# Kernel tuning notes

Hardware: AMD Instinct MI355X
Metric: run time of the kernel (lower is better)

## Reference

```python
import jax, jax.numpy as jnp
import numpy as np

D_MODEL = 1024
N_HEADS = 16
D_K = D_MODEL // N_HEADS


def setup_inputs() -> dict:
    key = jax.random.key(0)
    ks = jax.random.split(key, 11)
    B, S = 4, 2048
    scale = 1.0 / np.sqrt(D_MODEL)
    inp = {
        "Q": jax.random.normal(ks[0], (B, S, D_MODEL), jnp.float32),
        "K": jax.random.normal(ks[1], (B, S, D_MODEL), jnp.float32),
        "V": jax.random.normal(ks[2], (B, S, D_MODEL), jnp.float32),
        "Wq": jax.random.normal(ks[3], (D_MODEL, D_MODEL), jnp.float32) * scale,
        "bq": jnp.zeros((D_MODEL,), jnp.float32),
        "Wk": jax.random.normal(ks[4], (D_MODEL, D_MODEL), jnp.float32) * scale,
        "bk": jnp.zeros((D_MODEL,), jnp.float32),
        "Wv": jax.random.normal(ks[5], (D_MODEL, D_MODEL), jnp.float32) * scale,
        "bv": jnp.zeros((D_MODEL,), jnp.float32),
        "Wo": jax.random.normal(ks[6], (D_MODEL, D_MODEL), jnp.float32) * scale,
        "bo": jnp.zeros((D_MODEL,), jnp.float32),
    }
    return inp


def _split_heads(x):
    B, S, _ = x.shape
    return x.reshape(B, S, N_HEADS, D_K).transpose(0, 2, 1, 3)  # [B,H,S,Dk]


def reference(Q, K, V, Wq, bq, Wk, bk, Wv, bv, Wo, bo):
    # torch nn.Linear: y = x @ W.T + b
    q = _split_heads(Q @ Wq.T + bq)
    k = _split_heads(K @ Wk.T + bk)
    v = _split_heads(V @ Wv.T + bv)
    scores = jnp.einsum("bhsd,bhtd->bhst", q, k) / jnp.sqrt(jnp.float32(D_K))
    probs = jax.nn.softmax(scores, axis=-1)
    attn = jnp.einsum("bhst,bhtd->bhsd", probs, v)  # [B,H,S,Dk]
    B, H, S, Dk = attn.shape
    combined = attn.transpose(0, 2, 1, 3).reshape(B, S, H * Dk)
    return combined @ Wo.T + bo
```

## Files before the change

kernel.cpp:

```cpp
#include <hip/hip_runtime.h>
#include <hip/hip_bf16.h>

typedef float  f32x4  __attribute__((ext_vector_type(4)));
typedef float  f32x16 __attribute__((ext_vector_type(16)));
typedef float  fvec4  __attribute__((ext_vector_type(4)));
typedef __bf16 bf16x8 __attribute__((ext_vector_type(8)));
typedef unsigned short u16x4 __attribute__((ext_vector_type(4)));
typedef unsigned short u16x8 __attribute__((ext_vector_type(8)));
typedef unsigned int   u32x4 __attribute__((ext_vector_type(4)));

#define DEVINL __device__ __forceinline__

constexpr int D_MODEL = 1024;
constexpr int NH      = 16;
constexpr int DK      = 64;
constexpr int SEQ     = 2048;
constexpr int BATCH   = 4;
constexpr int M_TOK   = BATCH * SEQ;

DEVINL unsigned short f32_to_bf16_u(float f) {
    unsigned int u = __builtin_bit_cast(unsigned int, f);
    u = (u + 0x7FFFu + ((u >> 16) & 1u)) >> 16;
    return (unsigned short)u;
}

DEVINL float exp2_fast(float x) { return __builtin_amdgcn_exp2f(x); }

DEVINL unsigned cvt_pk_bf16(float lo, float hi_) {
    unsigned d;
    asm("v_cvt_pk_bf16_f32 %0, %1, %2" : "=v"(d) : "v"(lo), "v"(hi_));
    return d;
}

DEVINL int vperm_s(int s0) { return (s0 & ~12) | ((s0 & 4) << 1) | ((s0 & 8) >> 1); }

__global__ __launch_bounds__(256) void cvt4(const float* __restrict__ a,
                                            const float* __restrict__ b,
                                            const float* __restrict__ c,
                                            const float* __restrict__ d,
                                            unsigned short* __restrict__ dst, int n8)
{
    int y = blockIdx.y;
    const float* s = (y == 0) ? a : (y == 1) ? b : (y == 2) ? c : d;
    size_t i = blockIdx.x * 256 + threadIdx.x;
    fvec4 v0 = *reinterpret_cast<const fvec4*>(s + i * 8);
    fvec4 v1 = *reinterpret_cast<const fvec4*>(s + i * 8 + 4);
    bf16x8 o;
    #pragma unroll
    for (int j = 0; j < 4; ++j) { o[j] = (__bf16)v0[j]; o[j + 4] = (__bf16)v1[j]; }
    *reinterpret_cast<bf16x8*>(dst + ((size_t)y * n8 + i) * 8) = o;
}

__global__ __launch_bounds__(256) void gemm_qkv(
    const float* __restrict__ Qi, const float* __restrict__ Ki,
    const float* __restrict__ Vi,
    const unsigned short* __restrict__ wq, const unsigned short* __restrict__ wk,
    const unsigned short* __restrict__ wv,
    const float* __restrict__ bq, const float* __restrict__ bk,
    const float* __restrict__ bv,
    unsigned short* __restrict__ qo, unsigned short* __restrict__ ko,
    unsigned short* __restrict__ vo, float qscale)
{
    constexpr int K = D_MODEL;
    constexpr int BUF = 128 * 64 * 2;
    __shared__ char As_[BUF * 2];
    __shared__ char Bs_[BUF * 2];

    const int y = blockIdx.y;
    const float* Ap = (y == 0) ? Qi : (y == 1) ? Ki : Vi;
    const unsigned short* Wb = (y == 0) ? wq : (y == 1) ? wk : wv;
    const float* bias = (y == 0) ? bq : (y == 1) ? bk : bv;

    const int tid  = threadIdx.x;
    const int lane = tid & 63;
    const int wave = tid >> 6;
    const int wr = (wave >> 1) * 64;
    const int wc = (wave & 1) * 64;
    const int wg = ((int)blockIdx.x & 7) * 64 + ((int)blockIdx.x >> 3);
    const int n0 = (wg & 7) * 128;
    const int m0 = (wg >> 3) * 128;
    const int l15 = lane & 15, h16 = lane >> 4;

    f32x4 acc[4][4] = {};
    fvec4 ar[4][2];
    u16x8 wr_[4];

    #pragma unroll
    for (int i = 0; i < 4; ++i) {
        int chunk = tid + i * 256;
        int r = chunk >> 3, c16 = chunk & 7;
        const float* src = Ap + (size_t)(m0 + r) * K + c16 * 8;
        ar[i][0] = *reinterpret_cast<const fvec4*>(src);
        ar[i][1] = *reinterpret_cast<const fvec4*>(src + 4);
        wr_[i] = *reinterpret_cast<const u16x8*>(Wb + (size_t)(n0 + r) * K + c16 * 8);
    }
    #pragma unroll
    for (int i = 0; i < 4; ++i) {
        int chunk = tid + i * 256;
        int r = chunk >> 3;
        bf16x8 o;
        #pragma unroll
        for (int j = 0; j < 4; ++j) { o[j] = (__bf16)ar[i][0][j]; o[j + 4] = (__bf16)ar[i][1][j]; }
        int boff = (chunk * 16) ^ ((r & 7) << 4);
        *reinterpret_cast<bf16x8*>(As_ + boff) = o;
        *reinterpret_cast<u16x8*>(Bs_ + boff) = wr_[i];
    }
    __syncthreads();

    int curb = 0;
    for (int kt = 0; kt < K; kt += 64) {
        if (kt + 64 < K) {
            #pragma unroll
            for (int i = 0; i < 4; ++i) {
                int chunk = tid + i * 256;
                int r = chunk >> 3, c16 = chunk & 7;
                const float* src = Ap + (size_t)(m0 + r) * K + (kt + 64) + c16 * 8;
                ar[i][0] = *reinterpret_cast<const fvec4*>(src);
                ar[i][1] = *reinterpret_cast<const fvec4*>(src + 4);
                wr_[i] = *reinterpret_cast<const u16x8*>(Wb + (size_t)(n0 + r) * K + (kt + 64) + c16 * 8);
            }
        }

        const char* Ar = As_ + curb * BUF;
        const char* Br = Bs_ + curb * BUF;
        #pragma unroll
        for (int kk = 0; kk < 2; ++kk) {
            bf16x8 af[4], bfr[4];
            #pragma unroll
            for (int mi = 0; mi < 4; ++mi) {
                int r = wr + mi * 16 + l15;
                af[mi] = *reinterpret_cast<const bf16x8*>(
                    Ar + ((r * 128 + kk * 64 + h16 * 16) ^ ((r & 7) << 4)));
            }
            #pragma unroll
            for (int ni = 0; ni < 4; ++ni) {
                int r = wc + ni * 16 + l15;
                bfr[ni] = *reinterpret_cast<const bf16x8*>(
                    Br + ((r * 128 + kk * 64 + h16 * 16) ^ ((r & 7) << 4)));
            }
            #pragma unroll
            for (int mi = 0; mi < 4; ++mi)
                #pragma unroll
                for (int ni = 0; ni < 4; ++ni)
                    acc[mi][ni] = __builtin_amdgcn_mfma_f32_16x16x32_bf16(
                        af[mi], bfr[ni], acc[mi][ni], 0, 0, 0);
        }

        if (kt + 64 < K) {
            char* Aw = As_ + (curb ^ 1) * BUF;
            char* Bw = Bs_ + (curb ^ 1) * BUF;
            #pragma unroll
            for (int i = 0; i < 4; ++i) {
                int chunk = tid + i * 256;
                int r = chunk >> 3;
                bf16x8 o;
                #pragma unroll
                for (int j = 0; j < 4; ++j) { o[j] = (__bf16)ar[i][0][j]; o[j + 4] = (__bf16)ar[i][1][j]; }
                int boff = (chunk * 16) ^ ((r & 7) << 4);
                *reinterpret_cast<bf16x8*>(Aw + boff) = o;
                *reinterpret_cast<u16x8*>(Bw + boff) = wr_[i];
            }
        }
        __syncthreads();
        curb ^= 1;
    }

    const int rl = h16 * 4;
    #pragma unroll
    for (int mi = 0; mi < 4; ++mi) {
        #pragma unroll
        for (int ni = 0; ni < 4; ++ni) {
            int col = n0 + wc + ni * 16 + l15;
            float bv_ = bias[col];
            if (y == 2) {
                int row0 = m0 + wr + mi * 16 + rl;
                int bb = row0 >> 11, s0 = row0 & (SEQ - 1);
                int sp = vperm_s(s0);
                int h = col >> 6, dk = col & (DK - 1);
                u16x4 o;
                #pragma unroll
                for (int r = 0; r < 4; ++r)
                    o[r] = f32_to_bf16_u(acc[mi][ni][r] + bv_);
                *reinterpret_cast<u16x4*>(vo +
                    (((size_t)bb * NH + h) * DK + dk) * SEQ + sp) = o;
            } else {
                float sc = (y == 0) ? qscale : 1.0f;
                unsigned short* op = (y == 0) ? qo : ko;
                #pragma unroll
                for (int r = 0; r < 4; ++r) {
                    int row = m0 + wr + mi * 16 + rl + r;
                    int bb = row >> 11, s = row & (SEQ - 1);
                    int h = col >> 6, dk = col & (DK - 1);
                    op[((((size_t)bb * NH + h) * SEQ) + s) * DK + dk]
                        = f32_to_bf16_u((acc[mi][ni][r] + bv_) * sc);
                }
            }
        }
    }
}

__global__ __launch_bounds__(256) void gemm_obf(const unsigned short* __restrict__ Ap,
                                                const unsigned short* __restrict__ Wb,
                                                const float* __restrict__ bias,
                                                float* __restrict__ outp)
{
    constexpr int K = D_MODEL, N = D_MODEL;
    constexpr int BUF = 128 * 64 * 2;
    __shared__ char As_[BUF * 2];
    __shared__ char Bs_[BUF * 2];

    const int tid  = threadIdx.x;
    const int lane = tid & 63;
    const int wave = tid >> 6;
    const int wr = (wave >> 1) * 64;
    const int wc = (wave & 1) * 64;
    const int wg = ((int)blockIdx.x & 7) * 64 + ((int)blockIdx.x >> 3);
    const int n0 = (wg & 7) * 128;
    const int m0 = (wg >> 3) * 128;
    const int l15 = lane & 15, h16 = lane >> 4;

    f32x4 acc[4][4] = {};
    u16x8 areg[4], wreg[4];

    #pragma unroll
    for (int i = 0; i < 4; ++i) {
        int chunk = tid + i * 256;
        int r = chunk >> 3, c16 = chunk & 7;
        areg[i] = *reinterpret_cast<const u16x8*>(Ap + (size_t)(m0 + r) * K + c16 * 8);
        wreg[i] = *reinterpret_cast<const u16x8*>(Wb + (size_t)(n0 + r) * K + c16 * 8);
    }
    #pragma unroll
    for (int i = 0; i < 4; ++i) {
        int chunk = tid + i * 256;
        int r = chunk >> 3;
        int boff = (chunk * 16) ^ ((r & 7) << 4);
        *reinterpret_cast<u16x8*>(As_ + boff) = areg[i];
        *reinterpret_cast<u16x8*>(Bs_ + boff) = wreg[i];
    }
    __syncthreads();

    int curb = 0;
    for (int kt = 0; kt < K; kt += 64) {
        if (kt + 64 < K) {
            #pragma unroll
            for (int i = 0; i < 4; ++i) {
                int chunk = tid + i * 256;
                int r = chunk >> 3, c16 = chunk & 7;
                areg[i] = *reinterpret_cast<const u16x8*>(Ap + (size_t)(m0 + r) * K + (kt + 64) + c16 * 8);
                wreg[i] = *reinterpret_cast<const u16x8*>(Wb + (size_t)(n0 + r) * K + (kt + 64) + c16 * 8);
            }
        }

        const char* Ar = As_ + curb * BUF;
        const char* Br = Bs_ + curb * BUF;
        #pragma unroll
        for (int kk = 0; kk < 2; ++kk) {
            bf16x8 af[4], bfr[4];
            #pragma unroll
            for (int mi = 0; mi < 4; ++mi) {
                int r = wr + mi * 16 + l15;
                af[mi] = *reinterpret_cast<const bf16x8*>(
                    Ar + ((r * 128 + kk * 64 + h16 * 16) ^ ((r & 7) << 4)));
            }
            #pragma unroll
            for (int ni = 0; ni < 4; ++ni) {
                int r = wc + ni * 16 + l15;
                bfr[ni] = *reinterpret_cast<const bf16x8*>(
                    Br + ((r * 128 + kk * 64 + h16 * 16) ^ ((r & 7) << 4)));
            }
            #pragma unroll
            for (int mi = 0; mi < 4; ++mi)
                #pragma unroll
                for (int ni = 0; ni < 4; ++ni)
                    acc[mi][ni] = __builtin_amdgcn_mfma_f32_16x16x32_bf16(
                        af[mi], bfr[ni], acc[mi][ni], 0, 0, 0);
        }

        if (kt + 64 < K) {
            char* Aw = As_ + (curb ^ 1) * BUF;
            char* Bw = Bs_ + (curb ^ 1) * BUF;
            #pragma unroll
            for (int i = 0; i < 4; ++i) {
                int chunk = tid + i * 256;
                int r = chunk >> 3;
                int boff = (chunk * 16) ^ ((r & 7) << 4);
                *reinterpret_cast<u16x8*>(Aw + boff) = areg[i];
                *reinterpret_cast<u16x8*>(Bw + boff) = wreg[i];
            }
        }
        __syncthreads();
        curb ^= 1;
    }

    const int rl = h16 * 4;
    #pragma unroll
    for (int mi = 0; mi < 4; ++mi) {
        #pragma unroll
        for (int ni = 0; ni < 4; ++ni) {
            int col = n0 + wc + ni * 16 + l15;
            float bv = bias[col];
            #pragma unroll
            for (int r = 0; r < 4; ++r) {
                int row = m0 + wr + mi * 16 + rl + r;
                outp[(size_t)row * N + col] = acc[mi][ni][r] + bv;
            }
        }
    }
}

__global__ __launch_bounds__(512, 4) void attn_kernel(const unsigned short* __restrict__ qb,
                                                      const unsigned short* __restrict__ kb,
                                                      const unsigned short* __restrict__ vt,
                                                      unsigned short* __restrict__ ob)
{
    __shared__ char lds[32768];

    const int tid  = threadIdx.x;
    const int lane = tid & 63;
    const int tl31 = lane & 31;
    const int hi   = lane >> 5;
    const int wave = tid >> 6;
    const int wg   = ((int)blockIdx.x & 7) * 64 + ((int)blockIdx.x >> 3);
    const int bh   = wg >> 3;
    const int q0   = (wg & 7) * 256;
    const size_t base  = (size_t)bh * SEQ * DK;
    const size_t baseT = (size_t)bh * DK * SEQ;

    const int k_kt = tid >> 8, k_kd = (tid >> 6) & 3, k_hi = (tid >> 5) & 1, k_tl = tid & 31;
    const size_t k_goff = base + (size_t)(k_kt * 32 + k_tl) * DK + k_kd * 16 + k_hi * 8;
    const int v_tg = tid >> 6, v_dh = (tid >> 5) & 1, v_dl = tid & 31;
    const size_t v_goff = baseT + (size_t)(v_dh * 32 + v_dl) * SEQ + v_tg * 8;

    bf16x8 qf[4];
    #pragma unroll
    for (int kd = 0; kd < 4; ++kd)
        qf[kd] = *reinterpret_cast<const bf16x8*>(
            qb + base + (size_t)(q0 + wave * 32 + tl31) * DK + kd * 16 + hi * 8);

    f32x16 oaccT[2] = {};
    float l_run = 0.f;

    {
        u16x8 kreg = *reinterpret_cast<const u16x8*>(kb + k_goff);
        u16x8 vreg = *reinterpret_cast<const u16x8*>(vt + v_goff);
        *reinterpret_cast<u16x8*>(lds + tid * 16) = kreg;
        *reinterpret_cast<u16x8*>(lds + 8192 + tid * 16) = vreg;
    }
    __syncthreads();

    for (int t = 0; t < 32; ++t) {
        const int cur = t & 1;
        const char* Kr = lds + cur * 16384;
        const char* Vr = Kr + 8192;

        u16x8 kreg, vreg;
        if (t < 31) {
            const int t0n = (t + 1) * 64;
            kreg = *reinterpret_cast<const u16x8*>(kb + k_goff + (size_t)t0n * DK);
            vreg = *reinterpret_cast<const u16x8*>(vt + v_goff + t0n);
        }

        f32x16 sT[2] = {};
        __builtin_amdgcn_s_setprio(1);
        #pragma unroll
        for (int kt = 0; kt < 2; ++kt)
            #pragma unroll
            for (int kd = 0; kd < 4; ++kd) {
                bf16x8 kf = *reinterpret_cast<const bf16x8*>(Kr + kt * 4096 + kd * 1024 + lane * 16);
                sT[kt] = __builtin_amdgcn_mfma_f32_32x32x16_bf16(kf, qf[kd], sT[kt], 0, 0, 0);
            }
        __builtin_amdgcn_s_setprio(0);

        {
            float rs0 = 0.f, rs1 = 0.f, rs2 = 0.f, rs3 = 0.f;
            #pragma unroll
            for (int kt = 0; kt < 2; ++kt)
                #pragma unroll
                for (int i = 0; i < 16; i += 4) {
                    float p0 = exp2_fast(sT[kt][i + 0]);
                    float p1 = exp2_fast(sT[kt][i + 1]);
                    float p2 = exp2_fast(sT[kt][i + 2]);
                    float p3 = exp2_fast(sT[kt][i + 3]);
                    sT[kt][i + 0] = p0; sT[kt][i + 1] = p1;
                    sT[kt][i + 2] = p2; sT[kt][i + 3] = p3;
                    rs0 += p0; rs1 += p1; rs2 += p2; rs3 += p3;
                }
            float rs = (rs0 + rs1) + (rs2 + rs3);
            rs += __shfl_xor(rs, 32);
            l_run += rs;
        }

        __builtin_amdgcn_s_setprio(1);
        #pragma unroll
        for (int ks = 0; ks < 4; ++ks) {
            bf16x8 vfA0 = *reinterpret_cast<const bf16x8*>(Vr + ks * 2048 + hi * 1024 + tl31 * 16);
            bf16x8 vfA1 = *reinterpret_cast<const bf16x8*>(Vr + ks * 2048 + hi * 1024 + 512 + tl31 * 16);
            const int kt = ks >> 1, r0 = (ks & 1) * 8;
            u32x4 w;
            w[0] = cvt_pk_bf16(sT[kt][r0 + 0], sT[kt][r0 + 1]);
            w[1] = cvt_pk_bf16(sT[kt][r0 + 2], sT[kt][r0 + 3]);
            w[2] = cvt_pk_bf16(sT[kt][r0 + 4], sT[kt][r0 + 5]);
            w[3] = cvt_pk_bf16(sT[kt][r0 + 6], sT[kt][r0 + 7]);
            bf16x8 pa = __builtin_bit_cast(bf16x8, w);
            oaccT[0] = __builtin_amdgcn_mfma_f32_32x32x16_bf16(vfA0, pa, oaccT[0], 0, 0, 0);
            oaccT[1] = __builtin_amdgcn_mfma_f32_32x32x16_bf16(vfA1, pa, oaccT[1], 0, 0, 0);
        }
        __builtin_amdgcn_s_setprio(0);

        if (t < 31) {
            char* Kw = lds + (cur ^ 1) * 16384;
            *reinterpret_cast<u16x8*>(Kw + tid * 16) = kreg;
            *reinterpret_cast<u16x8*>(Kw + 8192 + tid * 16) = vreg;
        }
        __syncthreads();
    }

    char* myregion = lds + wave * 4096;
    const int bb = bh >> 4, h = bh & 15;
    {
        float rl = 1.0f / l_run;
        #pragma unroll
        for (int dh = 0; dh < 2; ++dh)
            #pragma unroll
            for (int r = 0; r < 16; ++r) {
                int dl = (r & 3) + 8 * (r >> 2) + 4 * hi + 32 * dh;
                int boff = (tl31 * 128 + dl * 2) ^ ((tl31 & 7) << 4);
                *reinterpret_cast<unsigned short*>(myregion + boff) =
                    f32_to_bf16_u(oaccT[dh][r] * rl);
            }
        #pragma unroll
        for (int c = 0; c < 4; ++c) {
            int chunk = lane + c * 64;
            int row = chunk >> 3, c16 = chunk & 7;
            int boff = (row * 128 + c16 * 16) ^ ((row & 7) << 4);
            u16x8 v = *reinterpret_cast<const u16x8*>(myregion + boff);
            size_t tok = (size_t)(bb * SEQ) + q0 + wave * 32 + row;
            *reinterpret_cast<u16x8*>(ob + tok * D_MODEL + h * DK + c16 * 8) = v;
        }
    }
}

extern "C" void kernel_launch(void* const* d_in, const int* in_sizes, int n_in,
                              void* d_out, int out_size, void* d_ws, size_t ws_size,
                              hipStream_t stream)
{
    const float* Q  = (const float*)d_in[0];
    const float* K_ = (const float*)d_in[1];
    const float* V  = (const float*)d_in[2];
    const float* Wq = (const float*)d_in[3];
    const float* bq = (const float*)d_in[4];
    const float* Wk = (const float*)d_in[5];
    const float* bk = (const float*)d_in[6];
    const float* Wv = (const float*)d_in[7];
    const float* bv = (const float*)d_in[8];
    const float* Wo = (const float*)d_in[9];
    const float* bo = (const float*)d_in[10];
    float* out = (float*)d_out;

    const size_t SZ = (size_t)M_TOK * D_MODEL;
    const size_t WZ = (size_t)D_MODEL * D_MODEL;
    unsigned short* qh_ = (unsigned short*)d_ws;
    unsigned short* kh_ = qh_ + SZ;
    unsigned short* vh_ = kh_ + SZ;
    unsigned short* ah_ = vh_ + SZ;
    unsigned short* wqb = ah_ + SZ;
    unsigned short* wkb = wqb + WZ;
    unsigned short* wvb = wkb + WZ;
    unsigned short* wob = wvb + WZ;

    const float qscale = 0.125f * 1.4426950408889634f;

    cvt4<<<dim3((int)(WZ / 8 / 256), 4), 256, 0, stream>>>(Wq, Wk, Wv, Wo, wqb, (int)(WZ / 8));

    gemm_qkv<<<dim3(512, 3), 256, 0, stream>>>(
        Q, K_, V, wqb, wkb, wvb, bq, bk, bv, qh_, kh_, vh_, qscale);
    attn_kernel<<<512, 512, 0, stream>>>(qh_, kh_, vh_, ah_);
    gemm_obf<<<512, 256, 0, stream>>>(ah_, wob, bo, out);
}
```

Before: 179.9 us.

## Deepen GEMM prefetch to two register stages ahead in QKV and output projections

Both projection GEMM kernels now keep two register sets of prefetched tiles, so global loads are issued two k-tiles ahead of the compute instead of one. This gives each global load more time to arrive before its data is written to shared memory. The loop is unrolled by two with fixed buffer roles. In exchange it raises register pressure, especially in the QKV kernel, where fp32 activations are staged in registers, and that may lower occupancy.

Result: slower. 217.2 us (+20.7%).

```diff
diff --git a/kernel.cpp b/kernel.cpp
--- a/kernel.cpp
+++ b/kernel.cpp
@@ -82,47 +82,34 @@
     const int l15 = lane & 15, h16 = lane >> 4;
 
     f32x4 acc[4][4] = {};
-    fvec4 ar[4][2];
-    u16x8 wr_[4];
-
-    #pragma unroll
-    for (int i = 0; i < 4; ++i) {
-        int chunk = tid + i * 256;
-        int r = chunk >> 3, c16 = chunk & 7;
-        const float* src = Ap + (size_t)(m0 + r) * K + c16 * 8;
-        ar[i][0] = *reinterpret_cast<const fvec4*>(src);
-        ar[i][1] = *reinterpret_cast<const fvec4*>(src + 4);
-        wr_[i] = *reinterpret_cast<const u16x8*>(Wb + (size_t)(n0 + r) * K + c16 * 8);
-    }
-    #pragma unroll
-    for (int i = 0; i < 4; ++i) {
-        int chunk = tid + i * 256;
-        int r = chunk >> 3;
-        bf16x8 o;
-        #pragma unroll
-        for (int j = 0; j < 4; ++j) { o[j] = (__bf16)ar[i][0][j]; o[j + 4] = (__bf16)ar[i][1][j]; }
-        int boff = (chunk * 16) ^ ((r & 7) << 4);
-        *reinterpret_cast<bf16x8*>(As_ + boff) = o;
-        *reinterpret_cast<u16x8*>(Bs_ + boff) = wr_[i];
-    }
-    __syncthreads();
-
-    int curb = 0;
-    for (int kt = 0; kt < K; kt += 64) {
-        if (kt + 64 < K) {
-            #pragma unroll
-            for (int i = 0; i < 4; ++i) {
-                int chunk = tid + i * 256;
-                int r = chunk >> 3, c16 = chunk & 7;
-                const float* src = Ap + (size_t)(m0 + r) * K + (kt + 64) + c16 * 8;
-                ar[i][0] = *reinterpret_cast<const fvec4*>(src);
-                ar[i][1] = *reinterpret_cast<const fvec4*>(src + 4);
-                wr_[i] = *reinterpret_cast<const u16x8*>(Wb + (size_t)(n0 + r) * K + (kt + 64) + c16 * 8);
-            }
-        }
-
-        const char* Ar = As_ + curb * BUF;
-        const char* Br = Bs_ + curb * BUF;
+    fvec4 aX[4][2]; u16x8 wX[4];
+    fvec4 aY[4][2]; u16x8 wY[4];
+
+    auto load_set = [&](fvec4 (&ar)[4][2], u16x8 (&wr2)[4], int kt) {
+        #pragma unroll
+        for (int i = 0; i < 4; ++i) {
+            int chunk = tid + i * 256;
+            int r = chunk >> 3, c16 = chunk & 7;
+            const float* src = Ap + (size_t)(m0 + r) * K + kt + c16 * 8;
+            ar[i][0] = *reinterpret_cast<const fvec4*>(src);
+            ar[i][1] = *reinterpret_cast<const fvec4*>(src + 4);
+            wr2[i] = *reinterpret_cast<const u16x8*>(Wb + (size_t)(n0 + r) * K + kt + c16 * 8);
+        }
+    };
+    auto write_set = [&](fvec4 (&ar)[4][2], u16x8 (&wr2)[4], char* Aw, char* Bw) {
+        #pragma unroll
+        for (int i = 0; i < 4; ++i) {
+            int chunk = tid + i * 256;
+            int r = chunk >> 3;
+            bf16x8 o;
+            #pragma unroll
+            for (int j = 0; j < 4; ++j) { o[j] = (__bf16)ar[i][0][j]; o[j + 4] = (__bf16)ar[i][1][j]; }
+            int boff = (chunk * 16) ^ ((r & 7) << 4);
+            *reinterpret_cast<bf16x8*>(Aw + boff) = o;
+            *reinterpret_cast<u16x8*>(Bw + boff) = wr2[i];
+        }
+    };
+    auto compute_buf = [&](const char* Ar, const char* Br) {
         #pragma unroll
         for (int kk = 0; kk < 2; ++kk) {
             bf16x8 af[4], bfr[4];
@@ -145,24 +132,22 @@
                     acc[mi][ni] = __builtin_amdgcn_mfma_f32_16x16x32_bf16(
                         af[mi], bfr[ni], acc[mi][ni], 0, 0, 0);
         }
-
-        if (kt + 64 < K) {
-            char* Aw = As_ + (curb ^ 1) * BUF;
-            char* Bw = Bs_ + (curb ^ 1) * BUF;
-            #pragma unroll
-            for (int i = 0; i < 4; ++i) {
-                int chunk = tid + i * 256;
-                int r = chunk >> 3;
-                bf16x8 o;
-                #pragma unroll
-                for (int j = 0; j < 4; ++j) { o[j] = (__bf16)ar[i][0][j]; o[j + 4] = (__bf16)ar[i][1][j]; }
-                int boff = (chunk * 16) ^ ((r & 7) << 4);
-                *reinterpret_cast<bf16x8*>(Aw + boff) = o;
-                *reinterpret_cast<u16x8*>(Bw + boff) = wr_[i];
-            }
-        }
+    };
+
+    load_set(aX, wX, 0);
+    write_set(aX, wX, As_, Bs_);
+    load_set(aY, wY, 64);
+    __syncthreads();
+
+    for (int t2 = 0; t2 < 16; t2 += 2) {
+        if (t2 + 2 < 16) load_set(aX, wX, (t2 + 2) * 64);
+        compute_buf(As_, Bs_);
+        write_set(aY, wY, As_ + BUF, Bs_ + BUF);
         __syncthreads();
-        curb ^= 1;
+        if (t2 + 3 < 16) load_set(aY, wY, (t2 + 3) * 64);
+        compute_buf(As_ + BUF, Bs_ + BUF);
+        if (t2 + 2 < 16) write_set(aX, wX, As_, Bs_);
+        __syncthreads();
     }
 
     const int rl = h16 * 4;
@@ -220,39 +205,29 @@
     const int l15 = lane & 15, h16 = lane >> 4;
 
     f32x4 acc[4][4] = {};
-    u16x8 areg[4], wreg[4];
-
-    #pragma unroll
-    for (int i = 0; i < 4; ++i) {
-        int chunk = tid + i * 256;
-        int r = chunk >> 3, c16 = chunk & 7;
-        areg[i] = *reinterpret_cast<const u16x8*>(Ap + (size_t)(m0 + r) * K + c16 * 8);
-        wreg[i] = *reinterpret_cast<const u16x8*>(Wb + (size_t)(n0 + r) * K + c16 * 8);
-    }
-    #pragma unroll
-    for (int i = 0; i < 4; ++i) {
-        int chunk = tid + i * 256;
-        int r = chunk >> 3;
-        int boff = (chunk * 16) ^ ((r & 7) << 4);
-        *reinterpret_cast<u16x8*>(As_ + boff) = areg[i];
-        *reinterpret_cast<u16x8*>(Bs_ + boff) = wreg[i];
-    }
-    __syncthreads();
-
-    int curb = 0;
-    for (int kt = 0; kt < K; kt += 64) {
-        if (kt + 64 < K) {
-            #pragma unroll
-            for (int i = 0; i < 4; ++i) {
-                int chunk = tid + i * 256;
-                int r = chunk >> 3, c16 = chunk & 7;
-                areg[i] = *reinterpret_cast<const u16x8*>(Ap + (size_t)(m0 + r) * K + (kt + 64) + c16 * 8);
-                wreg[i] = *reinterpret_cast<const u16x8*>(Wb + (size_t)(n0 + r) * K + (kt + 64) + c16 * 8);
-            }
-        }
-
-        const char* Ar = As_ + curb * BUF;
-        const char* Br = Bs_ + curb * BUF;
+    u16x8 aX[4], wX[4];
+    u16x8 aY[4], wY[4];
+
+    auto load_set = [&](u16x8 (&ar)[4], u16x8 (&wr2)[4], int kt) {
+        #pragma unroll
+        for (int i = 0; i < 4; ++i) {
+            int chunk = tid + i * 256;
+            int r = chunk >> 3, c16 = chunk & 7;
+            ar[i]  = *reinterpret_cast<const u16x8*>(Ap + (size_t)(m0 + r) * K + kt + c16 * 8);
+            wr2[i] = *reinterpret_cast<const u16x8*>(Wb + (size_t)(n0 + r) * K + kt + c16 * 8);
+        }
+    };
+    auto write_set = [&](u16x8 (&ar)[4], u16x8 (&wr2)[4], char* Aw, char* Bw) {
+        #pragma unroll
+        for (int i = 0; i < 4; ++i) {
+            int chunk = tid + i * 256;
+            int r = chunk >> 3;
+            int boff = (chunk * 16) ^ ((r & 7) << 4);
+            *reinterpret_cast<u16x8*>(Aw + boff) = ar[i];
+            *reinterpret_cast<u16x8*>(Bw + boff) = wr2[i];
+        }
+    };
+    auto compute_buf = [&](const char* Ar, const char* Br) {
         #pragma unroll
         for (int kk = 0; kk < 2; ++kk) {
             bf16x8 af[4], bfr[4];
@@ -275,21 +250,22 @@
                     acc[mi][ni] = __builtin_amdgcn_mfma_f32_16x16x32_bf16(
                         af[mi], bfr[ni], acc[mi][ni], 0, 0, 0);
         }
-
-        if (kt + 64 < K) {
-            char* Aw = As_ + (curb ^ 1) * BUF;
-            char* Bw = Bs_ + (curb ^ 1) * BUF;
-            #pragma unroll
-            for (int i = 0; i < 4; ++i) {
-                int chunk = tid + i * 256;
-                int r = chunk >> 3;
-                int boff = (chunk * 16) ^ ((r & 7) << 4);
-                *reinterpret_cast<u16x8*>(Aw + boff) = areg[i];
-                *reinterpret_cast<u16x8*>(Bw + boff) = wreg[i];
-            }
-        }
+    };
+
+    load_set(aX, wX, 0);
+    write_set(aX, wX, As_, Bs_);
+    load_set(aY, wY, 64);
+    __syncthreads();
+
+    for (int t2 = 0; t2 < 16; t2 += 2) {
+        if (t2 + 2 < 16) load_set(aX, wX, (t2 + 2) * 64);
+        compute_buf(As_, Bs_);
+        write_set(aY, wY, As_ + BUF, Bs_ + BUF);
         __syncthreads();
-        curb ^= 1;
+        if (t2 + 3 < 16) load_set(aY, wY, (t2 + 3) * 64);
+        compute_buf(As_ + BUF, Bs_ + BUF);
+        if (t2 + 2 < 16) write_set(aX, wX, As_, Bs_);
+        __syncthreads();
     }
 
     const int rl = h16 * 4;
```
